# Performance work log

Hardware: AMD Instinct MI355X
Metric: run time of the kernel (lower is better)

Reference implementation:

```python
import jax, jax.numpy as jnp
import numpy as np


def setup_inputs() -> dict:
    key = jax.random.key(0)
    k1, k2, k3, k4 = jax.random.split(key, 4)
    B, T, D, HS = 4, 2048, 1024, 64
    x = jax.random.normal(k1, (B, T, D), dtype=jnp.float32)
    # nn.Linear(d_model, head_size, bias=False) weights: (head_size, d_model)
    s = 1.0 / np.sqrt(D)
    Wk = jax.random.normal(k2, (HS, D), dtype=jnp.float32) * s
    Wq = jax.random.normal(k3, (HS, D), dtype=jnp.float32) * s
    Wv = jax.random.normal(k4, (HS, D), dtype=jnp.float32) * s
    return {"x": x, "Wk": Wk, "Wq": Wq, "Wv": Wv}


def reference(x, Wk, Wq, Wv):
    # x: [B, T, D]; W*: [HS, D]
    B, T, D = x.shape
    HS = Wk.shape[0]
    k = jnp.einsum('btd,hd->bth', x, Wk)  # [B, T, HS]
    q = jnp.einsum('btd,hd->bth', x, Wq)
    v = jnp.einsum('btd,hd->bth', x, Wv)
    # FAITHFUL to source bug: scores / hs**(-0.5) == scores * sqrt(hs)
    scale = jnp.asarray(np.sqrt(HS), dtype=x.dtype)
    scores = jnp.einsum('bqh,bkh->bqk', q, k) * scale  # [B, T, T]
    causal = jnp.tril(jnp.ones((T, T), dtype=bool))
    scores = jnp.where(causal, scores, jnp.asarray(-jnp.inf, dtype=scores.dtype))
    att = jax.nn.softmax(scores, axis=-1)  # dropout p=0.0 -> identity
    out = jnp.einsum('bqk,bkh->bqh', att, v)  # [B, T, HS]
    return out
```

## Files before the change

### kernel.cpp

```cpp
#include <hip/hip_runtime.h>

#define TSEQ 2048
#define DDIM 1024
#define HSZ  64
#define NB   4
#define NROWS (NB * TSEQ)

typedef short bf16x8 __attribute__((ext_vector_type(8)));
typedef short s16x4  __attribute__((ext_vector_type(4)));
typedef float f32x4  __attribute__((ext_vector_type(4)));

#define MFMA16(a, b, c) __builtin_amdgcn_mfma_f32_16x16x32_bf16((a), (b), (c), 0, 0, 0)

__device__ inline void split_bf16(float f, short& hi, short& lo) {
    unsigned u = __builtin_bit_cast(unsigned, f);
    hi = (short)(u >> 16);
    float fh = __builtin_bit_cast(float, u & 0xffff0000u);
    float fl = f - fh;
    lo = (short)(__builtin_bit_cast(unsigned, fl) >> 16);
}

__global__ __launch_bounds__(256) void wsplit_kernel(
    const float* __restrict__ Wk, const float* __restrict__ Wq, const float* __restrict__ Wv,
    short* __restrict__ wbhi, short* __restrict__ wblo)
{
    int i = blockIdx.x * 256 + threadIdx.x;
    int off = i << 2;
    int which = off >> 16;
    int loc = off & 65535;
    const float* src = (which == 0) ? Wk : (which == 1) ? Wq : Wv;
    float4 v = *(const float4*)(src + loc);
    short h0,h1,h2,h3, l0,l1,l2,l3;
    split_bf16(v.x, h0, l0); split_bf16(v.y, h1, l1);
    split_bf16(v.z, h2, l2); split_bf16(v.w, h3, l3);
    *(s16x4*)(wbhi + off) = (s16x4){h0,h1,h2,h3};
    *(s16x4*)(wblo + off) = (s16x4){l0,l1,l2,l3};
}

__global__ __launch_bounds__(256) void proj_mfma(
    const float* __restrict__ x,
    const short* __restrict__ wbhi, const short* __restrict__ wblo,
    short* __restrict__ khi, short* __restrict__ klo,
    short* __restrict__ qhi, short* __restrict__ qlo,
    short* __restrict__ vthi, short* __restrict__ vtlo)
{
    __shared__ __align__(16) short xhi[32][72], xlo[32][72];
    __shared__ __align__(16) short whi[64][72], wlo[64][72];

    const int tid  = threadIdx.x;
    const int w    = tid >> 6;
    const int lane = tid & 63;
    const int g    = lane >> 4;
    const int c    = lane & 15;
    const int mode = blockIdx.y;
    const long rb  = (long)blockIdx.x * 32;

    const short* wsrch = wbhi + mode * 65536;
    const short* wsrcl = wblo + mode * 65536;

    f32x4 acc[2];
    acc[0] = 0; acc[1] = 0;

    const int rowoff = (w & 1) * 16;
    const int coloff = (w >> 1) * 32;

    for (int k0 = 0; k0 < DDIM; k0 += 64) {
        #pragma unroll
        for (int u = 0; u < 2; ++u) {
            int idx = tid + u * 256;
            int row = idx >> 4, c4 = (idx & 15) << 2;
            float4 xv = *(const float4*)(x + (rb + row) * DDIM + k0 + c4);
            short h0,h1,h2,h3, l0,l1,l2,l3;
            split_bf16(xv.x, h0, l0); split_bf16(xv.y, h1, l1);
            split_bf16(xv.z, h2, l2); split_bf16(xv.w, h3, l3);
            *(s16x4*)&xhi[row][c4] = (s16x4){h0,h1,h2,h3};
            *(s16x4*)&xlo[row][c4] = (s16x4){l0,l1,l2,l3};
        }
        #pragma unroll
        for (int u = 0; u < 2; ++u) {
            int idx = tid + u * 256;
            int row = idx >> 3, c8 = (idx & 7) << 3;
            *(bf16x8*)&whi[row][c8] = *(const bf16x8*)(wsrch + row * DDIM + k0 + c8);
            *(bf16x8*)&wlo[row][c8] = *(const bf16x8*)(wsrcl + row * DDIM + k0 + c8);
        }
        __syncthreads();

        #pragma unroll
        for (int kk = 0; kk < 2; ++kk) {
            bf16x8 ah = *(const bf16x8*)&xhi[rowoff + c][kk*32 + 8*g];
            bf16x8 al = *(const bf16x8*)&xlo[rowoff + c][kk*32 + 8*g];
            #pragma unroll
            for (int ct = 0; ct < 2; ++ct) {
                bf16x8 bh = *(const bf16x8*)&whi[coloff + ct*16 + c][kk*32 + 8*g];
                bf16x8 bl = *(const bf16x8*)&wlo[coloff + ct*16 + c][kk*32 + 8*g];
                acc[ct] = MFMA16(al, bh, acc[ct]);
                acc[ct] = MFMA16(ah, bl, acc[ct]);
                acc[ct] = MFMA16(ah, bh, acc[ct]);
            }
        }
        __syncthreads();
    }

    if (mode < 2) {
        short* oh = (mode == 0) ? khi : qhi;
        short* ol = (mode == 0) ? klo : qlo;
        const float sc = (mode == 0) ? 1.0f : 8.0f;
        #pragma unroll
        for (int ct = 0; ct < 2; ++ct) {
            #pragma unroll
            for (int r = 0; r < 4; ++r) {
                long row = rb + rowoff + 4*g + r;
                float vv = acc[ct][r] * sc;
                short h, lo2; split_bf16(vv, h, lo2);
                oh[row * HSZ + coloff + ct*16 + c] = h;
                ol[row * HSZ + coloff + ct*16 + c] = lo2;
            }
        }
    } else {
        #pragma unroll
        for (int ct = 0; ct < 2; ++ct) {
            #pragma unroll
            for (int r = 0; r < 4; ++r) {
                short h, lo2; split_bf16(acc[ct][r], h, lo2);
                whi[coloff + ct*16 + c][rowoff + 4*g + r] = h;
                wlo[coloff + ct*16 + c][rowoff + 4*g + r] = lo2;
            }
        }
        __syncthreads();
        int batch = (int)(rb >> 11);
        int t0    = (int)(rb & 2047);
        int d = tid >> 2, t8 = (tid & 3) << 3;
        long gofs = ((long)batch * HSZ + d) * TSEQ + t0 + t8;
        *(bf16x8*)(vthi + gofs) = *(const bf16x8*)&whi[d][t8];
        *(bf16x8*)(vtlo + gofs) = *(const bf16x8*)&wlo[d][t8];
    }
}

__global__ __launch_bounds__(256) void attn_mfma(
    const short* __restrict__ qhi, const short* __restrict__ qlo,
    const short* __restrict__ khi, const short* __restrict__ klo,
    const short* __restrict__ vthi, const short* __restrict__ vtlo,
    float* __restrict__ out)
{
    __shared__ __align__(16) short phi[4][16][72], plo[4][16][72];
    __shared__ float smax[4][16], lsum[4][16];
    __shared__ float obuf[3][16][65];

    const int tid  = threadIdx.x;
    const int w    = tid >> 6;
    const int lane = tid & 63;
    const int g    = lane >> 4;
    const int c    = lane & 15;
    const int bid  = blockIdx.x;
    const int batch = bid & 3;
    const int tile  = 127 - (bid >> 2);
    const int qb0   = tile << 4;
    const long bb   = (long)batch * TSEQ;

    bf16x8 qa[2][2];
    {
        const long qofs = (bb + qb0 + c) * HSZ;
        #pragma unroll
        for (int kk = 0; kk < 2; ++kk) {
            qa[kk][0] = *(const bf16x8*)(qhi + qofs + kk*32 + 8*g);
            qa[kk][1] = *(const bf16x8*)(qlo + qofs + kk*32 + 8*g);
        }
    }

    f32x4 oacc[4];
    #pragma unroll
    for (int dt = 0; dt < 4; ++dt) oacc[dt] = 0;
    float m[4], l[4];
    #pragma unroll
    for (int r = 0; r < 4; ++r) { m[r] = -1e30f; l[r] = 0.0f; }

    const int keylen = (tile + 1) << 4;
    const int nsteps = (keylen + 255) >> 8;

    for (int s = 0; s < nsteps; ++s) {
        const int jbw = (s << 8) + (w << 6);
        const bool active = (jbw <= qb0 + 15);

        f32x4 sa[4];
        float mx[4];
        #pragma unroll
        for (int r = 0; r < 4; ++r) mx[r] = -1e30f;

        if (active) {
            #pragma unroll
            for (int ct = 0; ct < 4; ++ct) sa[ct] = 0;
            #pragma unroll
            for (int kk = 0; kk < 2; ++kk) {
                bf16x8 kbh[4], kbl[4];
                #pragma unroll
                for (int ct = 0; ct < 4; ++ct) {
                    const long kofs = (bb + jbw + ct*16 + c) * HSZ + kk*32 + 8*g;
                    kbh[ct] = *(const bf16x8*)(khi + kofs);
                    kbl[ct] = *(const bf16x8*)(klo + kofs);
                }
                #pragma unroll
                for (int ct = 0; ct < 4; ++ct) {
                    sa[ct] = MFMA16(qa[kk][1], kbh[ct], sa[ct]);
                    sa[ct] = MFMA16(qa[kk][0], kbl[ct], sa[ct]);
                    sa[ct] = MFMA16(qa[kk][0], kbh[ct], sa[ct]);
                }
            }
            if (jbw + 63 > qb0) {
                #pragma unroll
                for (int ct = 0; ct < 4; ++ct) {
                    int key = jbw + ct*16 + c;
                    #pragma unroll
                    for (int r = 0; r < 4; ++r)
                        if (key > qb0 + 4*g + r) sa[ct][r] = -1e30f;
                }
            }
            #pragma unroll
            for (int r = 0; r < 4; ++r)
                mx[r] = fmaxf(fmaxf(sa[0][r], sa[1][r]), fmaxf(sa[2][r], sa[3][r]));
            #pragma unroll
            for (int off = 1; off <= 8; off <<= 1) {
                #pragma unroll
                for (int r = 0; r < 4; ++r)
                    mx[r] = fmaxf(mx[r], __shfl_xor(mx[r], off));
            }
        }
        if (c == 0) {
            #pragma unroll
            for (int r = 0; r < 4; ++r) smax[w][4*g + r] = mx[r];
        }
        __syncthreads();

        float mn[4];
        #pragma unroll
        for (int r = 0; r < 4; ++r) {
            float cm = fmaxf(fmaxf(smax[0][4*g+r], smax[1][4*g+r]),
                             fmaxf(smax[2][4*g+r], smax[3][4*g+r]));
            mn[r] = fmaxf(m[r], cm);
        }

        float rs[4] = {0.f, 0.f, 0.f, 0.f};
        if (active) {
            #pragma unroll
            for (int ct = 0; ct < 4; ++ct) {
                #pragma unroll
                for (int r = 0; r < 4; ++r) {
                    float p = __expf(sa[ct][r] - mn[r]);
                    sa[ct][r] = p;
                    rs[r] += p;
                }
            }
            #pragma unroll
            for (int off = 1; off <= 8; off <<= 1) {
                #pragma unroll
                for (int r = 0; r < 4; ++r) rs[r] += __shfl_xor(rs[r], off);
            }
            #pragma unroll
            for (int ct = 0; ct < 4; ++ct) {
                #pragma unroll
                for (int r = 0; r < 4; ++r) {
                    short h, lo2; split_bf16(sa[ct][r], h, lo2);
                    phi[w][4*g + r][ct*16 + c] = h;
                    plo[w][4*g + r][ct*16 + c] = lo2;
                }
            }
        }
        if (c == 0) {
            #pragma unroll
            for (int r = 0; r < 4; ++r) lsum[w][4*g + r] = rs[r];
        }
        __syncthreads();

        float fsc[4];
        #pragma unroll
        for (int r = 0; r < 4; ++r) {
            float rsum = lsum[0][4*g+r] + lsum[1][4*g+r] + lsum[2][4*g+r] + lsum[3][4*g+r];
            fsc[r] = __expf(m[r] - mn[r]);
            l[r] = l[r] * fsc[r] + rsum;
            m[r] = mn[r];
        }
        #pragma unroll
        for (int dt = 0; dt < 4; ++dt) {
            #pragma unroll
            for (int r = 0; r < 4; ++r) oacc[dt][r] *= fsc[r];
        }

        if (active) {
            #pragma unroll
            for (int kk = 0; kk < 2; ++kk) {
                bf16x8 pah = *(const bf16x8*)&phi[w][c][kk*32 + 8*g];
                bf16x8 pal = *(const bf16x8*)&plo[w][c][kk*32 + 8*g];
                bf16x8 vbh[4], vbl[4];
                #pragma unroll
                for (int dt = 0; dt < 4; ++dt) {
                    const long vofs = ((long)(batch*HSZ + dt*16 + c)) * TSEQ + jbw + kk*32 + 8*g;
                    vbh[dt] = *(const bf16x8*)(vthi + vofs);
                    vbl[dt] = *(const bf16x8*)(vtlo + vofs);
                }
                #pragma unroll
                for (int dt = 0; dt < 4; ++dt) {
                    oacc[dt] = MFMA16(pal, vbh[dt], oacc[dt]);
                    oacc[dt] = MFMA16(pah, vbl[dt], oacc[dt]);
                    oacc[dt] = MFMA16(pah, vbh[dt], oacc[dt]);
                }
            }
        }
    }

    if (w > 0) {
        #pragma unroll
        for (int dt = 0; dt < 4; ++dt) {
            #pragma unroll
            for (int r = 0; r < 4; ++r)
                obuf[w-1][4*g + r][dt*16 + c] = oacc[dt][r];
        }
    }
    __syncthreads();
    if (w == 0) {
        #pragma unroll
        for (int r = 0; r < 4; ++r) {
            float linv = 1.0f / l[r];
            #pragma unroll
            for (int dt = 0; dt < 4; ++dt) {
                float vv = oacc[dt][r] + obuf[0][4*g+r][dt*16+c]
                         + obuf[1][4*g+r][dt*16+c] + obuf[2][4*g+r][dt*16+c];
                out[(bb + qb0 + 4*g + r) * HSZ + dt*16 + c] = vv * linv;
            }
        }
    }
}

extern "C" void kernel_launch(void* const* d_in, const int* in_sizes, int n_in,
                              void* d_out, int out_size, void* d_ws, size_t ws_size,
                              hipStream_t stream) {
    const float* x  = (const float*)d_in[0];
    const float* Wk = (const float*)d_in[1];
    const float* Wq = (const float*)d_in[2];
    const float* Wv = (const float*)d_in[3];
    float* out = (float*)d_out;

    short* ws = (short*)d_ws;
    const size_t SEG = (size_t)NROWS * HSZ;
    short* khi  = ws;
    short* klo  = ws + SEG;
    short* qhi  = ws + 2*SEG;
    short* qlo  = ws + 3*SEG;
    short* vthi = ws + 4*SEG;
    short* vtlo = ws + 5*SEG;
    short* wbhi = ws + 6*SEG;
    short* wblo = wbhi + 3*HSZ*DDIM;

    wsplit_kernel<<<192, 256, 0, stream>>>(Wk, Wq, Wv, wbhi, wblo);
    proj_mfma<<<dim3(256, 3), 256, 0, stream>>>(x, wbhi, wblo,
                                                khi, klo, qhi, qlo, vthi, vtlo);
    attn_mfma<<<NB * (TSEQ / 16), 256, 0, stream>>>(qhi, qlo, khi, klo, vthi, vtlo, out);
}
```

Before: 151.9 us.

## Fuse QKV projection, use 8-wave attention with per-wave softmax and LDS-direct weight loads

The projection kernel now computes K, Q and V in one 512-thread block, so x is read and split once instead of three times. Weights are pre-swizzled and loaded straight into LDS with global_load_lds. Attention moves to 8 waves that each keep an independent online-softmax state, which removes the per-step block barriers, and the states are merged at the end. The change also remaps tiles to balance causal work across blocks and switches the bf16 hi/lo split to round-to-nearest. These changes aim to cut redundant x traffic and barrier stalls, at the cost of higher register and LDS pressure and a more complex final merge.

```diff
diff --git a/kernel.cpp b/kernel.cpp
--- a/kernel.cpp
+++ b/kernel.cpp
@@ -9,15 +9,23 @@
 typedef short bf16x8 __attribute__((ext_vector_type(8)));
 typedef short s16x4  __attribute__((ext_vector_type(4)));
 typedef float f32x4  __attribute__((ext_vector_type(4)));
+typedef unsigned int u32;
+typedef unsigned int u32x4 __attribute__((ext_vector_type(4)));
 
 #define MFMA16(a, b, c) __builtin_amdgcn_mfma_f32_16x16x32_bf16((a), (b), (c), 0, 0, 0)
 
-__device__ inline void split_bf16(float f, short& hi, short& lo) {
-    unsigned u = __builtin_bit_cast(unsigned, f);
-    hi = (short)(u >> 16);
-    float fh = __builtin_bit_cast(float, u & 0xffff0000u);
+__device__ inline void split_rn(float f, short& hi, short& lo) {
+    u32 u = __builtin_bit_cast(u32, f);
+    u32 rr = (u + 0x7fffu + ((u >> 16) & 1u)) & 0xffff0000u;
+    hi = (short)(rr >> 16);
+    float fh = __builtin_bit_cast(float, rr);
     float fl = f - fh;
-    lo = (short)(__builtin_bit_cast(unsigned, fl) >> 16);
+    lo = (short)(__builtin_bit_cast(u32, fl) >> 16);
+}
+
+__device__ inline void gload_lds16(const void* g, void* l) {
+    __builtin_amdgcn_global_load_lds((const __attribute__((address_space(1))) void*)g,
+                                     (__attribute__((address_space(3))) void*)l, 16, 0, 0);
 }
 
 __global__ __launch_bounds__(256) void wsplit_kernel(
@@ -30,14 +38,18 @@
     int loc = off & 65535;
     const float* src = (which == 0) ? Wk : (which == 1) ? Wq : Wv;
     float4 v = *(const float4*)(src + loc);
+    int row = off >> 10;
+    int k = off & 1023;
+    int kd = (k & ~63) | ((k & 63) ^ ((row & 7) << 3));
+    int dst = (row << 10) | kd;
     short h0,h1,h2,h3, l0,l1,l2,l3;
-    split_bf16(v.x, h0, l0); split_bf16(v.y, h1, l1);
-    split_bf16(v.z, h2, l2); split_bf16(v.w, h3, l3);
-    *(s16x4*)(wbhi + off) = (s16x4){h0,h1,h2,h3};
-    *(s16x4*)(wblo + off) = (s16x4){l0,l1,l2,l3};
-}
-
-__global__ __launch_bounds__(256) void proj_mfma(
+    split_rn(v.x, h0, l0); split_rn(v.y, h1, l1);
+    split_rn(v.z, h2, l2); split_rn(v.w, h3, l3);
+    *(s16x4*)(wbhi + dst) = (s16x4){h0,h1,h2,h3};
+    *(s16x4*)(wblo + dst) = (s16x4){l0,l1,l2,l3};
+}
+
+__global__ __launch_bounds__(512) void proj_mfma(
     const float* __restrict__ x,
     const short* __restrict__ wbhi, const short* __restrict__ wblo,
     short* __restrict__ khi, short* __restrict__ klo,
@@ -45,43 +57,37 @@
     short* __restrict__ vthi, short* __restrict__ vtlo)
 {
     __shared__ __align__(16) short xhi[32][72], xlo[32][72];
-    __shared__ __align__(16) short whi[64][72], wlo[64][72];
+    __shared__ __align__(16) short whi[192 * 64], wlo[192 * 64];
 
     const int tid  = threadIdx.x;
     const int w    = tid >> 6;
     const int lane = tid & 63;
     const int g    = lane >> 4;
     const int c    = lane & 15;
-    const int mode = blockIdx.y;
+    const int rowoff = (w & 1) * 16;
+    const int colgrp = w >> 1;
     const long rb  = (long)blockIdx.x * 32;
 
-    const short* wsrch = wbhi + mode * 65536;
-    const short* wsrcl = wblo + mode * 65536;
-
-    f32x4 acc[2];
-    acc[0] = 0; acc[1] = 0;
-
-    const int rowoff = (w & 1) * 16;
-    const int coloff = (w >> 1) * 32;
+    f32x4 acc[3];
+    acc[0] = 0; acc[1] = 0; acc[2] = 0;
 
     for (int k0 = 0; k0 < DDIM; k0 += 64) {
-        #pragma unroll
-        for (int u = 0; u < 2; ++u) {
-            int idx = tid + u * 256;
-            int row = idx >> 4, c4 = (idx & 15) << 2;
+        {
+            int row = tid >> 4, c4 = (tid & 15) << 2;
             float4 xv = *(const float4*)(x + (rb + row) * DDIM + k0 + c4);
             short h0,h1,h2,h3, l0,l1,l2,l3;
-            split_bf16(xv.x, h0, l0); split_bf16(xv.y, h1, l1);
-            split_bf16(xv.z, h2, l2); split_bf16(xv.w, h3, l3);
+            split_rn(xv.x, h0, l0); split_rn(xv.y, h1, l1);
+            split_rn(xv.z, h2, l2); split_rn(xv.w, h3, l3);
             *(s16x4*)&xhi[row][c4] = (s16x4){h0,h1,h2,h3};
             *(s16x4*)&xlo[row][c4] = (s16x4){l0,l1,l2,l3};
         }
         #pragma unroll
-        for (int u = 0; u < 2; ++u) {
-            int idx = tid + u * 256;
-            int row = idx >> 3, c8 = (idx & 7) << 3;
-            *(bf16x8*)&whi[row][c8] = *(const bf16x8*)(wsrch + row * DDIM + k0 + c8);
-            *(bf16x8*)&wlo[row][c8] = *(const bf16x8*)(wsrcl + row * DDIM + k0 + c8);
+        for (int u = 0; u < 3; ++u) {
+            int hchunk = w * 3 + u;
+            int sidx = hchunk * 512 + lane * 8;
+            int trow = sidx >> 6, tk = sidx & 63;
+            gload_lds16(wbhi + trow * DDIM + k0 + tk, whi + hchunk * 512);
+            gload_lds16(wblo + trow * DDIM + k0 + tk, wlo + hchunk * 512);
         }
         __syncthreads();
 
@@ -90,240 +96,223 @@
             bf16x8 ah = *(const bf16x8*)&xhi[rowoff + c][kk*32 + 8*g];
             bf16x8 al = *(const bf16x8*)&xlo[rowoff + c][kk*32 + 8*g];
             #pragma unroll
-            for (int ct = 0; ct < 2; ++ct) {
-                bf16x8 bh = *(const bf16x8*)&whi[coloff + ct*16 + c][kk*32 + 8*g];
-                bf16x8 bl = *(const bf16x8*)&wlo[coloff + ct*16 + c][kk*32 + 8*g];
-                acc[ct] = MFMA16(al, bh, acc[ct]);
-                acc[ct] = MFMA16(ah, bl, acc[ct]);
-                acc[ct] = MFMA16(ah, bh, acc[ct]);
+            for (int t = 0; t < 3; ++t) {
+                int wr = colgrp * 48 + t * 16 + c;
+                int koff = (kk*32 + 8*g) ^ ((wr & 7) << 3);
+                bf16x8 bh = *(const bf16x8*)&whi[wr * 64 + koff];
+                bf16x8 bl = *(const bf16x8*)&wlo[wr * 64 + koff];
+                acc[t] = MFMA16(al, bh, acc[t]);
+                acc[t] = MFMA16(ah, bl, acc[t]);
+                acc[t] = MFMA16(ah, bh, acc[t]);
             }
         }
         __syncthreads();
     }
 
-    if (mode < 2) {
-        short* oh = (mode == 0) ? khi : qhi;
-        short* ol = (mode == 0) ? klo : qlo;
-        const float sc = (mode == 0) ? 1.0f : 8.0f;
-        #pragma unroll
-        for (int ct = 0; ct < 2; ++ct) {
+    __syncthreads();
+    short (*vtrh)[36] = (short(*)[36])(&xhi[0][0]);
+    short (*vtrl)[36] = (short(*)[36])(&xlo[0][0]);
+    const int batch = (int)(rb >> 11);
+    const int t0 = (int)(rb & 2047);
+    #pragma unroll
+    for (int t = 0; t < 3; ++t) {
+        int col16 = colgrp * 48 + t * 16;
+        int mode = col16 >> 6;
+        int lcol = col16 - (mode << 6) + c;
+        if (mode < 2) {
+            short* oh = mode ? qhi : khi;
+            short* ol = mode ? qlo : klo;
+            const float sc = mode ? 8.0f : 1.0f;
             #pragma unroll
             for (int r = 0; r < 4; ++r) {
                 long row = rb + rowoff + 4*g + r;
-                float vv = acc[ct][r] * sc;
-                short h, lo2; split_bf16(vv, h, lo2);
-                oh[row * HSZ + coloff + ct*16 + c] = h;
-                ol[row * HSZ + coloff + ct*16 + c] = lo2;
-            }
-        }
-    } else {
-        #pragma unroll
-        for (int ct = 0; ct < 2; ++ct) {
+                short h, lo2; split_rn(acc[t][r] * sc, h, lo2);
+                oh[row * HSZ + lcol] = h;
+                ol[row * HSZ + lcol] = lo2;
+            }
+        } else {
             #pragma unroll
             for (int r = 0; r < 4; ++r) {
-                short h, lo2; split_bf16(acc[ct][r], h, lo2);
-                whi[coloff + ct*16 + c][rowoff + 4*g + r] = h;
-                wlo[coloff + ct*16 + c][rowoff + 4*g + r] = lo2;
-            }
-        }
-        __syncthreads();
-        int batch = (int)(rb >> 11);
-        int t0    = (int)(rb & 2047);
-        int d = tid >> 2, t8 = (tid & 3) << 3;
-        long gofs = ((long)batch * HSZ + d) * TSEQ + t0 + t8;
-        *(bf16x8*)(vthi + gofs) = *(const bf16x8*)&whi[d][t8];
-        *(bf16x8*)(vtlo + gofs) = *(const bf16x8*)&wlo[d][t8];
-    }
-}
-
-__global__ __launch_bounds__(256) void attn_mfma(
+                short h, lo2; split_rn(acc[t][r], h, lo2);
+                vtrh[lcol][rowoff + 4*g + r] = h;
+                vtrl[lcol][rowoff + 4*g + r] = lo2;
+            }
+        }
+    }
+    __syncthreads();
+    {
+        int d = tid >> 3, t4 = (tid & 7) << 2;
+        long gofs = ((long)(batch * HSZ + d)) * TSEQ + t0 + t4;
+        *(s16x4*)(vthi + gofs) = *(const s16x4*)&vtrh[d][t4];
+        *(s16x4*)(vtlo + gofs) = *(const s16x4*)&vtrl[d][t4];
+    }
+}
+
+__global__ __launch_bounds__(512, 4) void attn_mfma(
     const short* __restrict__ qhi, const short* __restrict__ qlo,
     const short* __restrict__ khi, const short* __restrict__ klo,
     const short* __restrict__ vthi, const short* __restrict__ vtlo,
     float* __restrict__ out)
 {
-    __shared__ __align__(16) short phi[4][16][72], plo[4][16][72];
-    __shared__ float smax[4][16], lsum[4][16];
-    __shared__ float obuf[3][16][65];
+    __shared__ __align__(16) u32  pbuf[8][16][68];
+    __shared__ float obuf[7][16][68];
+    __shared__ float mlbuf[8][16][2];
 
     const int tid  = threadIdx.x;
     const int w    = tid >> 6;
     const int lane = tid & 63;
     const int g    = lane >> 4;
     const int c    = lane & 15;
-    const int bid  = blockIdx.x;
-    const int batch = bid & 3;
-    const int tile  = 127 - (bid >> 2);
+
+    const int bid   = blockIdx.x;
+    const int work  = ((bid & 7) << 6) | (bid >> 3);
+    const int batch = work >> 7;
+    const int rank  = work & 127;
+    const int tile  = (rank < 64) ? (127 - 2*rank) : (126 - 2*(rank - 64));
     const int qb0   = tile << 4;
     const long bb   = (long)batch * TSEQ;
 
-    bf16x8 qa[2][2];
+    bf16x8 qh[2], ql[2];
     {
         const long qofs = (bb + qb0 + c) * HSZ;
         #pragma unroll
         for (int kk = 0; kk < 2; ++kk) {
-            qa[kk][0] = *(const bf16x8*)(qhi + qofs + kk*32 + 8*g);
-            qa[kk][1] = *(const bf16x8*)(qlo + qofs + kk*32 + 8*g);
+            qh[kk] = *(const bf16x8*)(qhi + qofs + kk*32 + 8*g);
+            ql[kk] = *(const bf16x8*)(qlo + qofs + kk*32 + 8*g);
         }
     }
 
     f32x4 oacc[4];
     #pragma unroll
     for (int dt = 0; dt < 4; ++dt) oacc[dt] = 0;
-    float m[4], l[4];
-    #pragma unroll
-    for (int r = 0; r < 4; ++r) { m[r] = -1e30f; l[r] = 0.0f; }
-
-    const int keylen = (tile + 1) << 4;
-    const int nsteps = (keylen + 255) >> 8;
-
-    for (int s = 0; s < nsteps; ++s) {
-        const int jbw = (s << 8) + (w << 6);
-        const bool active = (jbw <= qb0 + 15);
-
-        f32x4 sa[4];
-        float mx[4];
-        #pragma unroll
-        for (int r = 0; r < 4; ++r) mx[r] = -1e30f;
-
-        if (active) {
-            #pragma unroll
-            for (int ct = 0; ct < 4; ++ct) sa[ct] = 0;
+    float m = -1e30f, l = 0.0f;
+
+    const int lastkey = qb0 + 15;
+    if (64 * w <= lastkey) {
+        const int nsteps = ((lastkey - 64 * w) >> 9) + 1;
+        for (int s = 0; s < nsteps; ++s) {
+            const int jb = (s << 9) + (w << 6);
+            f32x4 sa[4];
+            sa[0] = 0; sa[1] = 0; sa[2] = 0; sa[3] = 0;
             #pragma unroll
             for (int kk = 0; kk < 2; ++kk) {
-                bf16x8 kbh[4], kbl[4];
-                #pragma unroll
-                for (int ct = 0; ct < 4; ++ct) {
-                    const long kofs = (bb + jbw + ct*16 + c) * HSZ + kk*32 + 8*g;
-                    kbh[ct] = *(const bf16x8*)(khi + kofs);
-                    kbl[ct] = *(const bf16x8*)(klo + kofs);
-                }
-                #pragma unroll
-                for (int ct = 0; ct < 4; ++ct) {
-                    sa[ct] = MFMA16(qa[kk][1], kbh[ct], sa[ct]);
-                    sa[ct] = MFMA16(qa[kk][0], kbl[ct], sa[ct]);
-                    sa[ct] = MFMA16(qa[kk][0], kbh[ct], sa[ct]);
-                }
-            }
-            if (jbw + 63 > qb0) {
-                #pragma unroll
-                for (int ct = 0; ct < 4; ++ct) {
-                    int key = jbw + ct*16 + c;
+                bf16x8 kb_h[4], kb_l[4];
+                #pragma unroll
+                for (int t = 0; t < 4; ++t) {
+                    const long kofs = (bb + jb + t*16 + c) * HSZ + kk*32 + 8*g;
+                    kb_h[t] = *(const bf16x8*)(khi + kofs);
+                    kb_l[t] = *(const bf16x8*)(klo + kofs);
+                }
+                #pragma unroll
+                for (int t = 0; t < 4; ++t) {
+                    sa[t] = MFMA16(kb_h[t], ql[kk], sa[t]);
+                    sa[t] = MFMA16(kb_l[t], qh[kk], sa[t]);
+                    sa[t] = MFMA16(kb_h[t], qh[kk], sa[t]);
+                }
+            }
+            if (jb + 63 > qb0) {
+                #pragma unroll
+                for (int t = 0; t < 4; ++t) {
+                    const int kb0 = jb + t*16 + 4*g;
                     #pragma unroll
                     for (int r = 0; r < 4; ++r)
-                        if (key > qb0 + 4*g + r) sa[ct][r] = -1e30f;
-                }
-            }
-            #pragma unroll
-            for (int r = 0; r < 4; ++r)
-                mx[r] = fmaxf(fmaxf(sa[0][r], sa[1][r]), fmaxf(sa[2][r], sa[3][r]));
-            #pragma unroll
-            for (int off = 1; off <= 8; off <<= 1) {
-                #pragma unroll
-                for (int r = 0; r < 4; ++r)
-                    mx[r] = fmaxf(mx[r], __shfl_xor(mx[r], off));
-            }
-        }
-        if (c == 0) {
-            #pragma unroll
-            for (int r = 0; r < 4; ++r) smax[w][4*g + r] = mx[r];
-        }
-        __syncthreads();
-
-        float mn[4];
-        #pragma unroll
-        for (int r = 0; r < 4; ++r) {
-            float cm = fmaxf(fmaxf(smax[0][4*g+r], smax[1][4*g+r]),
-                             fmaxf(smax[2][4*g+r], smax[3][4*g+r]));
-            mn[r] = fmaxf(m[r], cm);
-        }
-
-        float rs[4] = {0.f, 0.f, 0.f, 0.f};
-        if (active) {
-            #pragma unroll
-            for (int ct = 0; ct < 4; ++ct) {
+                        if (kb0 + r > qb0 + c) sa[t][r] = -1e30f;
+                }
+            }
+            float mx = sa[0][0];
+            #pragma unroll
+            for (int t = 0; t < 4; ++t)
+                #pragma unroll
+                for (int r = 0; r < 4; ++r) mx = fmaxf(mx, sa[t][r]);
+            mx = fmaxf(mx, __shfl_xor(mx, 16));
+            mx = fmaxf(mx, __shfl_xor(mx, 32));
+            const float mn = fmaxf(m, mx);
+            float rs = 0.0f;
+            #pragma unroll
+            for (int t = 0; t < 4; ++t) {
                 #pragma unroll
                 for (int r = 0; r < 4; ++r) {
-                    float p = __expf(sa[ct][r] - mn[r]);
-                    sa[ct][r] = p;
-                    rs[r] += p;
-                }
-            }
-            #pragma unroll
-            for (int off = 1; off <= 8; off <<= 1) {
-                #pragma unroll
-                for (int r = 0; r < 4; ++r) rs[r] += __shfl_xor(rs[r], off);
-            }
-            #pragma unroll
-            for (int ct = 0; ct < 4; ++ct) {
-                #pragma unroll
-                for (int r = 0; r < 4; ++r) {
-                    short h, lo2; split_bf16(sa[ct][r], h, lo2);
-                    phi[w][4*g + r][ct*16 + c] = h;
-                    plo[w][4*g + r][ct*16 + c] = lo2;
-                }
-            }
-        }
-        if (c == 0) {
-            #pragma unroll
-            for (int r = 0; r < 4; ++r) lsum[w][4*g + r] = rs[r];
-        }
-        __syncthreads();
-
-        float fsc[4];
-        #pragma unroll
-        for (int r = 0; r < 4; ++r) {
-            float rsum = lsum[0][4*g+r] + lsum[1][4*g+r] + lsum[2][4*g+r] + lsum[3][4*g+r];
-            fsc[r] = __expf(m[r] - mn[r]);
-            l[r] = l[r] * fsc[r] + rsum;
-            m[r] = mn[r];
-        }
-        #pragma unroll
-        for (int dt = 0; dt < 4; ++dt) {
-            #pragma unroll
-            for (int r = 0; r < 4; ++r) oacc[dt][r] *= fsc[r];
-        }
-
-        if (active) {
+                    float p = __expf(sa[t][r] - mn);
+                    rs += p;
+                    short h, lo2; split_rn(p, h, lo2);
+                    pbuf[w][c][t*16 + 4*g + r] =
+                        (u32)(unsigned short)h | ((u32)(unsigned short)lo2 << 16);
+                }
+            }
+            rs += __shfl_xor(rs, 16);
+            rs += __shfl_xor(rs, 32);
+            const float fs = __expf(m - mn);
+            l = l * fs + rs;
+            m = mn;
+            float fr[4];
+            #pragma unroll
+            for (int r = 0; r < 4; ++r) fr[r] = __shfl(fs, (g << 4) + 4*g + r);
+            #pragma unroll
+            for (int dt = 0; dt < 4; ++dt) {
+                oacc[dt][0] *= fr[0]; oacc[dt][1] *= fr[1];
+                oacc[dt][2] *= fr[2]; oacc[dt][3] *= fr[3];
+            }
             #pragma unroll
             for (int kk = 0; kk < 2; ++kk) {
-                bf16x8 pah = *(const bf16x8*)&phi[w][c][kk*32 + 8*g];
-                bf16x8 pal = *(const bf16x8*)&plo[w][c][kk*32 + 8*g];
-                bf16x8 vbh[4], vbl[4];
+                u32x4 pw0 = *(const u32x4*)&pbuf[w][c][kk*32 + 8*g];
+                u32x4 pw1 = *(const u32x4*)&pbuf[w][c][kk*32 + 8*g + 4];
+                u32x4 th, tl;
+                th[0] = (pw0[0] & 0xffffu) | (pw0[1] << 16);
+                tl[0] = (pw0[0] >> 16)    | (pw0[1] & 0xffff0000u);
+                th[1] = (pw0[2] & 0xffffu) | (pw0[3] << 16);
+                tl[1] = (pw0[2] >> 16)    | (pw0[3] & 0xffff0000u);
+                th[2] = (pw1[0] & 0xffffu) | (pw1[1] << 16);
+                tl[2] = (pw1[0] >> 16)    | (pw1[1] & 0xffff0000u);
+                th[3] = (pw1[2] & 0xffffu) | (pw1[3] << 16);
+                tl[3] = (pw1[2] >> 16)    | (pw1[3] & 0xffff0000u);
+                bf16x8 pah = __builtin_bit_cast(bf16x8, th);
+                bf16x8 pal = __builtin_bit_cast(bf16x8, tl);
+                bf16x8 vb_h[4], vb_l[4];
                 #pragma unroll
                 for (int dt = 0; dt < 4; ++dt) {
-                    const long vofs = ((long)(batch*HSZ + dt*16 + c)) * TSEQ + jbw + kk*32 + 8*g;
-                    vbh[dt] = *(const bf16x8*)(vthi + vofs);
-                    vbl[dt] = *(const bf16x8*)(vtlo + vofs);
+                    const long vofs = ((long)(batch * HSZ + dt*16 + c)) * TSEQ + jb + kk*32 + 8*g;
+                    vb_h[dt] = *(const bf16x8*)(vthi + vofs);
+                    vb_l[dt] = *(const bf16x8*)(vtlo + vofs);
                 }
                 #pragma unroll
                 for (int dt = 0; dt < 4; ++dt) {
-                    oacc[dt] = MFMA16(pal, vbh[dt], oacc[dt]);
-                    oacc[dt] = MFMA16(pah, vbl[dt], oacc[dt]);
-                    oacc[dt] = MFMA16(pah, vbh[dt], oacc[dt]);
-                }
-            }
-        }
-    }
-
+                    oacc[dt] = MFMA16(pal, vb_h[dt], oacc[dt]);
+                    oacc[dt] = MFMA16(pah, vb_l[dt], oacc[dt]);
+                    oacc[dt] = MFMA16(pah, vb_h[dt], oacc[dt]);
+                }
+            }
+        }
+    }
+
+    if (lane < 16) { mlbuf[w][lane][0] = m; mlbuf[w][lane][1] = l; }
     if (w > 0) {
         #pragma unroll
-        for (int dt = 0; dt < 4; ++dt) {
+        for (int dt = 0; dt < 4; ++dt)
             #pragma unroll
             for (int r = 0; r < 4; ++r)
                 obuf[w-1][4*g + r][dt*16 + c] = oacc[dt][r];
-        }
     }
     __syncthreads();
     if (w == 0) {
         #pragma unroll
         for (int r = 0; r < 4; ++r) {
-            float linv = 1.0f / l[r];
+            const int row = 4*g + r;
+            float ms = mlbuf[0][row][0];
+            #pragma unroll
+            for (int wv = 1; wv < 8; ++wv) ms = fmaxf(ms, mlbuf[wv][row][0]);
+            float ls = 0.0f; float fw[8];
+            #pragma unroll
+            for (int wv = 0; wv < 8; ++wv) {
+                fw[wv] = __expf(mlbuf[wv][row][0] - ms);
+                ls += mlbuf[wv][row][1] * fw[wv];
+            }
+            const float linv = 1.0f / ls;
             #pragma unroll
             for (int dt = 0; dt < 4; ++dt) {
-                float vv = oacc[dt][r] + obuf[0][4*g+r][dt*16+c]
-                         + obuf[1][4*g+r][dt*16+c] + obuf[2][4*g+r][dt*16+c];
-                out[(bb + qb0 + 4*g + r) * HSZ + dt*16 + c] = vv * linv;
+                float val = oacc[dt][r] * fw[0];
+                #pragma unroll
+                for (int wv = 1; wv < 8; ++wv) val += obuf[wv-1][row][dt*16 + c] * fw[wv];
+                out[(bb + qb0 + row) * HSZ + dt*16 + c] = val * linv;
             }
         }
     }
@@ -350,7 +339,6 @@
     short* wblo = wbhi + 3*HSZ*DDIM;
 
     wsplit_kernel<<<192, 256, 0, stream>>>(Wk, Wq, Wv, wbhi, wblo);
-    proj_mfma<<<dim3(256, 3), 256, 0, stream>>>(x, wbhi, wblo,
-                                                khi, klo, qhi, qlo, vthi, vtlo);
-    attn_mfma<<<NB * (TSEQ / 16), 256, 0, stream>>>(qhi, qlo, khi, klo, vthi, vtlo, out);
-}
+    proj_mfma<<<256, 512, 0, stream>>>(x, wbhi, wblo, khi, klo, qhi, qlo, vthi, vtlo);
+    attn_mfma<<<512, 512, 0, stream>>>(qhi, qlo, khi, klo, vthi, vtlo, out);
+}
```

After: 148.8 us. 1.02x faster.
